# Optimization experiments

Hardware: AMD Instinct MI355X
Metric: run time of the kernel (lower is better)

The kernel has to match this reference:

```python
import jax, jax.numpy as jnp
import numpy as np

B, S, D, VOCAB = 64, 2048, 256, 288

def setup_inputs() -> dict:
    key = jax.random.key(0)
    k1, k2, k3 = jax.random.split(key, 3)
    TE = jax.random.randint(k1, (B, S, 2), 0, VOCAB, dtype=jnp.int64)
    W1 = jax.random.normal(k2, (VOCAB + 7, D), dtype=jnp.float32) * 0.05
    b1 = jnp.zeros((D,), dtype=jnp.float32)
    W2 = jax.random.normal(k3, (D, D), dtype=jnp.float32) * 0.05
    b2 = jnp.zeros((D,), dtype=jnp.float32)
    return {"TE": TE, "T": VOCAB, "W1": W1, "b1": b1, "W2": W2, "b2": b2}

def reference(TE, T, W1, b1, W2, b2):
    # one_hot(day,7)||one_hot(time,T) @ W1  ==  gather rows of W1 and add
    day = TE[..., 0].astype(jnp.int32) % 7          # [B, S]
    tod = TE[..., 1].astype(jnp.int32) % T          # [B, S]
    h = W1[day] + W1[7 + tod] + b1                  # [B, S, D]  (Linear 1)
    h = jax.nn.relu(h)
    out = jnp.einsum('bsd,de->bse', h, W2) + b2     # [B, S, D]  (Linear 2)
    return out[:, :, None, :]                       # [B, S, 1, D]
```

## Files before the change

### kernel.cpp

```cpp
#include <hip/hip_runtime.h>
#include <hip/hip_bf16.h>


typedef __bf16 bf16x4 __attribute__((ext_vector_type(4)));
typedef __bf16 bf16x8 __attribute__((ext_vector_type(8)));
typedef float  f32x4  __attribute__((ext_vector_type(4)));

#define M_TOTAL   131072
#define BM        128


__global__ __launch_bounds__(256) void prep_w2s(const float* __restrict__ W2,
                                                __bf16* __restrict__ W2S,
                                                const int* __restrict__ TE32,
                                                int* __restrict__ flag) {
    int c = blockIdx.x * 256 + threadIdx.x;
    if (c < 8192) {
        int lane = c & 63;
        int ksnt = c >> 6;
        int ks = ksnt & 7, nt = ksnt >> 3;
        int n  = nt * 16 + (lane & 15);
        int k0 = ks * 32 + (lane >> 4) * 8;
        bf16x8 w;
#pragma unroll
        for (int j = 0; j < 8; ++j) w[j] = (__bf16)W2[(k0 + j) * 256 + n];
        *(bf16x8*)(W2S + c * 8) = w;
    }
    if (blockIdx.x == 0 && threadIdx.x < 64) {
        int v = 0;
        for (int i = (int)threadIdx.x; i < 2048; i += 64) v |= TE32[2 * i + 1];
        unsigned long long nz = __ballot(v != 0);
        if (threadIdx.x == 0) *flag = (nz == 0ull) ? 1 : 0;
    }
}

__global__ __launch_bounds__(256, 2) void temb_gemm(
        const int*  __restrict__ TE32,
        const int*  __restrict__ Tp,
        const float* __restrict__ W1,
        const float* __restrict__ b1,
        const __bf16* __restrict__ W2S,
        const float* __restrict__ b2,
        const int*  __restrict__ flag,
        float* __restrict__ out)
{
    __shared__ __bf16 h_lds[BM * 256];

    const int T    = Tp[0];
    const int is64 = *flag;
    const int wave = threadIdx.x >> 6;
    const int lane = threadIdx.x & 63;
    const int m    = lane & 15;
    const int quad = lane >> 4;
    const int rowBase = blockIdx.x * BM + wave * 32;

    const f32x4 b1v = *(const f32x4*)(b1 + lane * 4);

    int dayv = 0, todv = 0;
    if (lane < 32) {
        if (is64) {
            const int4 te = *(const int4*)(TE32 + 4 * (rowBase + lane));
            dayv = te.x; todv = te.z;
        } else {
            const int2 te = *(const int2*)(TE32 + 2 * (rowBase + lane));
            dayv = te.x; todv = te.y;
        }
        dayv %= 7; todv %= T;
    }

    const int hbase = wave * 32 * 256;
#pragma unroll 4
    for (int r = 0; r < 32; ++r) {
        const int day = __builtin_amdgcn_readfirstlane(__shfl(dayv, r));
        const int tod = __builtin_amdgcn_readfirstlane(__shfl(todv, r));
        const f32x4 a = *(const f32x4*)(W1 + day * 256 + lane * 4);
        const f32x4 b = *(const f32x4*)(W1 + (7 + tod) * 256 + lane * 4);
        bf16x4 hv;
#pragma unroll
        for (int j = 0; j < 4; ++j)
            hv[j] = (__bf16)fmaxf(a[j] + b[j] + b1v[j], 0.0f);
        *(bf16x4*)(h_lds + hbase + r * 256 + lane * 4) = hv;
    }
    __syncthreads();

    bf16x8 afrag[2][8];
#pragma unroll
    for (int t = 0; t < 2; ++t)
#pragma unroll
        for (int ks = 0; ks < 8; ++ks)
            afrag[t][ks] = *(const bf16x8*)(h_lds + hbase + (t * 16 + m) * 256
                                            + ks * 32 + quad * 8);

    float b2r[16];
#pragma unroll
    for (int nt = 0; nt < 16; ++nt) b2r[nt] = b2[nt * 16 + m];

    const __bf16* __restrict__ wp = W2S + lane * 8;
#pragma unroll 4
    for (int nt = 0; nt < 16; ++nt) {
        f32x4 acc0 = {0.f, 0.f, 0.f, 0.f};
        f32x4 acc1 = {0.f, 0.f, 0.f, 0.f};
#pragma unroll
        for (int ks = 0; ks < 8; ++ks) {
            bf16x8 bfrag = *(const bf16x8*)(wp + (nt * 8 + ks) * 512);
            acc0 = __builtin_amdgcn_mfma_f32_16x16x32_bf16(afrag[0][ks], bfrag, acc0, 0, 0, 0);
            acc1 = __builtin_amdgcn_mfma_f32_16x16x32_bf16(afrag[1][ks], bfrag, acc1, 0, 0, 0);
        }
        const int ncol = nt * 16 + m;
        const float bias = b2r[nt];
#pragma unroll
        for (int r = 0; r < 4; ++r) {
            const int row0 = rowBase + quad * 4 + r;
            out[row0 * 256 + ncol]        = acc0[r] + bias;
            out[(row0 + 16) * 256 + ncol] = acc1[r] + bias;
        }
    }
}

extern "C" void kernel_launch(void* const* d_in, const int* in_sizes, int n_in,
                              void* d_out, int out_size, void* d_ws, size_t ws_size,
                              hipStream_t stream) {
    const int*   TE = (const int*)  d_in[0];
    const int*   Tp = (const int*)  d_in[1];
    const float* W1 = (const float*)d_in[2];
    const float* b1 = (const float*)d_in[3];
    const float* W2 = (const float*)d_in[4];
    const float* b2 = (const float*)d_in[5];
    __bf16* W2S  = (__bf16*)d_ws;
    int*    flag = (int*)((char*)d_ws + 131072);
    float*  out  = (float*)d_out;

    prep_w2s<<<32, 256, 0, stream>>>(W2, W2S, TE, flag);
    temb_gemm<<<M_TOTAL / BM, 256, 0, stream>>>(TE, Tp, W1, b1, W2S, b2, flag, out);
}
```

Baseline: 165.3 us.

## Precompute relu(W1 pair sums) table and gather bf16 rows per token

A prep kernel now builds a 7*T-row bf16 table holding relu(W1[day]+W1[7+tod]+b1) for every (day, tod) pair, alongside the W2 swizzle. The GEMM kernel then gathers one precomputed row per token instead of loading two fp32 W1 rows and doing the add and relu. The shared buffer shrinks to a per-wave 16-row padded staging area, which allows a launch bound of 4 blocks per CU. T is now taken from the W1 input size on the host instead of being read from device memory. This adds a larger prep launch (about 2000 small blocks) and a ~1MB table, and it relies on in_sizes being element counts.

New measurement: 178.2 us. 7.8% more time.

```diff
diff --git a/kernel.cpp b/kernel.cpp
--- a/kernel.cpp
+++ b/kernel.cpp
@@ -8,88 +8,91 @@
 
 #define M_TOTAL   131072
 #define BM        128
+#define HPAD      258
 
 
-__global__ __launch_bounds__(256) void prep_w2s(const float* __restrict__ W2,
-                                                __bf16* __restrict__ W2S,
-                                                const int* __restrict__ TE32,
-                                                int* __restrict__ flag) {
-    int c = blockIdx.x * 256 + threadIdx.x;
-    if (c < 8192) {
-        int lane = c & 63;
-        int ksnt = c >> 6;
-        int ks = ksnt & 7, nt = ksnt >> 3;
-        int n  = nt * 16 + (lane & 15);
-        int k0 = ks * 32 + (lane >> 4) * 8;
-        bf16x8 w;
+__global__ __launch_bounds__(64) void prep_all(const float* __restrict__ W1,
+                                               const float* __restrict__ b1,
+                                               const float* __restrict__ W2,
+                                               __bf16* __restrict__ W2S,
+                                               __bf16* __restrict__ Htab,
+                                               const int* __restrict__ TE32,
+                                               int* __restrict__ flag, int T) {
+    const int b = blockIdx.x, lane = threadIdx.x;
+    const int nTab = 7 * T;
+    if (b < nTab) {
+        const float* __restrict__ wa = W1 + (b / T) * 256;
+        const float* __restrict__ wb = W1 + (7 + b % T) * 256;
+        f32x4 a = *(const f32x4*)(wa + lane * 4);
+        f32x4 c = *(const f32x4*)(wb + lane * 4);
+        f32x4 d = *(const f32x4*)(b1 + lane * 4);
+        bf16x4 h;
 #pragma unroll
-        for (int j = 0; j < 8; ++j) w[j] = (__bf16)W2[(k0 + j) * 256 + n];
-        *(bf16x8*)(W2S + c * 8) = w;
-    }
-    if (blockIdx.x == 0 && threadIdx.x < 64) {
-        int v = 0;
-        for (int i = (int)threadIdx.x; i < 2048; i += 64) v |= TE32[2 * i + 1];
-        unsigned long long nz = __ballot(v != 0);
-        if (threadIdx.x == 0) *flag = (nz == 0ull) ? 1 : 0;
+        for (int j = 0; j < 4; ++j) h[j] = (__bf16)fmaxf(a[j] + c[j] + d[j], 0.0f);
+        *(bf16x4*)(Htab + b * 256 + lane * 4) = h;
+    } else {
+        const int wb = b - nTab;
+#pragma unroll
+        for (int q = 0; q < 2; ++q) {
+            int c = (wb * 64 + lane) * 2 + q;
+            int l = c & 63, ksnt = c >> 6;
+            int ks = ksnt & 7, nt = ksnt >> 3;
+            int n  = nt * 16 + (l & 15);
+            int k0 = ks * 32 + (l >> 4) * 8;
+            bf16x8 w;
+#pragma unroll
+            for (int j = 0; j < 8; ++j) w[j] = (__bf16)W2[(k0 + j) * 256 + n];
+            *(bf16x8*)(W2S + c * 8) = w;
+        }
+        if (wb == 0) {
+            int v = 0;
+            for (int i = lane; i < 2048; i += 64) v |= TE32[2 * i + 1];
+            unsigned long long nz = __ballot(v != 0);
+            if (lane == 0) *flag = (nz == 0ull) ? 1 : 0;
+        }
     }
 }
 
-__global__ __launch_bounds__(256, 2) void temb_gemm(
-        const int*  __restrict__ TE32,
-        const int*  __restrict__ Tp,
-        const float* __restrict__ W1,
-        const float* __restrict__ b1,
+__global__ __launch_bounds__(256, 4) void temb_gemm(
+        const int*   __restrict__ TE32,
+        const __bf16* __restrict__ Htab,
         const __bf16* __restrict__ W2S,
         const float* __restrict__ b2,
-        const int*  __restrict__ flag,
-        float* __restrict__ out)
+        const int*   __restrict__ flag,
+        float* __restrict__ out, int T)
 {
-    __shared__ __bf16 h_lds[BM * 256];
-
-    const int T    = Tp[0];
+    __shared__ __bf16 hbuf[4][16 * HPAD];
     const int is64 = *flag;
     const int wave = threadIdx.x >> 6;
     const int lane = threadIdx.x & 63;
     const int m    = lane & 15;
     const int quad = lane >> 4;
+    const int half = lane >> 5;
+    const int c32  = lane & 31;
     const int rowBase = blockIdx.x * BM + wave * 32;
+    __bf16* __restrict__ myH = &hbuf[wave][0];
 
-    const f32x4 b1v = *(const f32x4*)(b1 + lane * 4);
-
-    int dayv = 0, todv = 0;
+    int code = 0;
     if (lane < 32) {
-        if (is64) {
-            const int4 te = *(const int4*)(TE32 + 4 * (rowBase + lane));
-            dayv = te.x; todv = te.z;
-        } else {
-            const int2 te = *(const int2*)(TE32 + 2 * (rowBase + lane));
-            dayv = te.x; todv = te.y;
-        }
-        dayv %= 7; todv %= T;
+        int day, tod;
+        if (is64) { int4 te = *(const int4*)(TE32 + 4 * (rowBase + lane)); day = te.x; tod = te.z; }
+        else      { int2 te = *(const int2*)(TE32 + 2 * (rowBase + lane)); day = te.x; tod = te.y; }
+        code = (day % 7) * T + tod % T;
     }
-
-    const int hbase = wave * 32 * 256;
-#pragma unroll 4
-    for (int r = 0; r < 32; ++r) {
-        const int day = __builtin_amdgcn_readfirstlane(__shfl(dayv, r));
-        const int tod = __builtin_amdgcn_readfirstlane(__shfl(todv, r));
-        const f32x4 a = *(const f32x4*)(W1 + day * 256 + lane * 4);
-        const f32x4 b = *(const f32x4*)(W1 + (7 + tod) * 256 + lane * 4);
-        bf16x4 hv;
-#pragma unroll
-        for (int j = 0; j < 4; ++j)
-            hv[j] = (__bf16)fmaxf(a[j] + b[j] + b1v[j], 0.0f);
-        *(bf16x4*)(h_lds + hbase + r * 256 + lane * 4) = hv;
-    }
-    __syncthreads();
 
     bf16x8 afrag[2][8];
 #pragma unroll
-    for (int t = 0; t < 2; ++t)
+    for (int t = 0; t < 2; ++t) {
+#pragma unroll
+        for (int g = 0; g < 8; ++g) {
+            const int ridx = __shfl(code, t * 16 + 2 * g + half);
+            bf16x8 hv = *(const bf16x8*)(Htab + ridx * 256 + c32 * 8);
+            *(bf16x8*)(myH + (2 * g + half) * HPAD + c32 * 8) = hv;
+        }
 #pragma unroll
         for (int ks = 0; ks < 8; ++ks)
-            afrag[t][ks] = *(const bf16x8*)(h_lds + hbase + (t * 16 + m) * 256
-                                            + ks * 32 + quad * 8);
+            afrag[t][ks] = *(const bf16x8*)(myH + m * HPAD + ks * 32 + quad * 8);
+    }
 
     float b2r[16];
 #pragma unroll
@@ -121,15 +124,17 @@
                               void* d_out, int out_size, void* d_ws, size_t ws_size,
                               hipStream_t stream) {
     const int*   TE = (const int*)  d_in[0];
-    const int*   Tp = (const int*)  d_in[1];
     const float* W1 = (const float*)d_in[2];
     const float* b1 = (const float*)d_in[3];
     const float* W2 = (const float*)d_in[4];
     const float* b2 = (const float*)d_in[5];
+    const int T = in_sizes[2] / 256 - 7;
+
     __bf16* W2S  = (__bf16*)d_ws;
-    int*    flag = (int*)((char*)d_ws + 131072);
+    __bf16* Htab = (__bf16*)((char*)d_ws + 131072);
+    int*    flag = (int*)((char*)d_ws + 131072 + (size_t)7 * T * 256 * 2);
     float*  out  = (float*)d_out;
 
-    prep_w2s<<<32, 256, 0, stream>>>(W2, W2S, TE, flag);
-    temb_gemm<<<M_TOTAL / BM, 256, 0, stream>>>(TE, Tp, W1, b1, W2S, b2, flag, out);
+    prep_all<<<7 * T + 64, 64, 0, stream>>>(W1, b1, W2, W2S, Htab, TE, flag, T);
+    temb_gemm<<<M_TOTAL / BM, 256, 0, stream>>>(TE, Htab, W2S, b2, flag, out, T);
 }
```
